# Optimization experiments

Hardware: AMD Instinct MI355X
Metric: run time of the kernel (lower is better)

Reference implementation:

```python
import jax, jax.numpy as jnp
import numpy as np

B = 256            # user batch size
D = 64             # embedding_dim
NR_USERS = 100000
NR_ITEMS = 10000
HID = 32


def _mlp_params(key, in_dim):
    # Keras Dense default: glorot_uniform weights, zero bias
    dims = [in_dim, HID, HID, HID, 1]
    ws, bs = [], []
    for i in range(4):
        key, k = jax.random.split(key)
        lim = np.sqrt(6.0 / (dims[i] + dims[i + 1])).astype(np.float32)
        ws.append(jax.random.uniform(k, (dims[i], dims[i + 1]), jnp.float32, -lim, lim))
        bs.append(jnp.zeros((dims[i + 1],), jnp.float32))
    return ws, bs


def setup_inputs() -> dict:
    key = jax.random.key(0)
    ks = jax.random.split(key, 6)
    users = jax.random.randint(ks[0], (B,), 0, NR_USERS)
    user_emb = jax.random.normal(ks[1], (NR_USERS, D), jnp.float32)
    item_emb = jax.random.normal(ks[2], (NR_ITEMS, D), jnp.float32)
    inp = {"users": users, "user_emb": user_emb, "item_emb": item_emb}
    for name, k, in_dim in (("l", ks[3], 2 * D), ("r", ks[4], 2 * D), ("p", ks[5], D)):
        ws, bs = _mlp_params(k, in_dim)
        for i in range(4):
            inp[f"{name}w{i}"] = ws[i]
            inp[f"{name}b{i}"] = bs[i]
    return inp


def _pair_head(eu, ie, ws, bs):
    # Faithful to: concat([tile(eu),[1,I,1]], tile(ie,[B,1,1])) @ W0 + b0
    # concat @ W0 == eu @ W0[:D] + ie @ W0[D:]  (avoids materializing [B,I,2D])
    h = jax.nn.relu((eu @ ws[0][:D])[:, None, :] + (ie @ ws[0][D:])[None, :, :] + bs[0])
    h = jax.nn.relu(h @ ws[1] + bs[1])
    h = jax.nn.relu(h @ ws[2] + bs[2])
    return jax.nn.sigmoid(h @ ws[3] + bs[3])[..., 0]  # [B, I]


def _item_head(x, ws, bs):
    h = jax.nn.relu(x @ ws[0] + bs[0])
    h = jax.nn.relu(h @ ws[1] + bs[1])
    h = jax.nn.relu(h @ ws[2] + bs[2])
    return jax.nn.sigmoid(h @ ws[3] + bs[3])[..., 0]  # [I]


def reference(users, user_emb, item_emb,
              lw0, lb0, lw1, lb1, lw2, lb2, lw3, lb3,
              rw0, rb0, rw1, rb1, rw2, rb2, rw3, rb3,
              pw0, pb0, pw1, pb1, pw2, pb2, pw3, pb3):
    eu = user_emb[users]  # [B, D]
    likes = _pair_head(eu, item_emb, [lw0, lw1, lw2, lw3], [lb0, lb1, lb2, lb3])
    rated = _pair_head(eu, item_emb, [rw0, rw1, rw2, rw3], [rb0, rb1, rb2, rb3])
    popular = _item_head(item_emb, [pw0, pw1, pw2, pw3], [pb0, pb1, pb2, pb3])
    # tf.keras.losses.cosine_similarity returns NEGATIVE cosine similarity,
    # so sim = (1 + (-cos)) / 2 = (1 - cos) / 2
    n = eu * jax.lax.rsqrt(jnp.maximum(jnp.sum(eu * eu, -1, keepdims=True), 1e-12))
    cos = n @ n.T  # [B, B]
    user_sim = (1.0 - cos) / 2.0
    return likes, user_sim, rated, popular
```

## Files before the change

### kernel.cpp

```cpp
#include <hip/hip_runtime.h>
#include <hip/hip_bf16.h>

#define NB 256
#define D 64
#define NI 10000

typedef __attribute__((ext_vector_type(8))) short bf16x8;
typedef __attribute__((ext_vector_type(16))) float f32x16;

union PK8 { unsigned u[4]; bf16x8 v; };

static constexpr int WS_AL  = 0;
static constexpr int WS_AR  = 8192;
static constexpr int WS_N   = 16384;
static constexpr int WS_CL  = 32768;
static constexpr int WS_CR  = 352768;
static constexpr int WS_TAB = 672768;

static constexpr long OUT_LIKES = 0;
static constexpr long OUT_SIM   = 2560000;
static constexpr long OUT_RATED = 2625536;
static constexpr long OUT_POP   = 5185536;

__device__ __forceinline__ unsigned pkbf(float a, float b) {
    unsigned r;
    asm("v_cvt_pk_bf16_f32 %0, %1, %2" : "=v"(r) : "v"(a), "v"(b));
    return r;
}
__device__ __forceinline__ float relu(float x) { return fmaxf(x, 0.f); }

struct A4 { float4 a0, a1, a2, a3; };
__device__ __forceinline__ A4 ldA(const float* p) {
    A4 r;
    r.a0 = *(const float4*)p;        r.a1 = *(const float4*)(p + 4);
    r.a2 = *(const float4*)(p + 16); r.a3 = *(const float4*)(p + 20);
    return r;
}

__global__ __launch_bounds__(256) void k_prep(
        const int* __restrict__ users, const float* __restrict__ uemb,
        const float* __restrict__ iemb,
        const float* __restrict__ lw0, const float* __restrict__ lb0,
        const float* __restrict__ rw0, const float* __restrict__ rb0,
        const float* __restrict__ lw1, const float* __restrict__ lb1,
        const float* __restrict__ lw2, const float* __restrict__ lb2,
        const float* __restrict__ lw3, const float* __restrict__ lb3,
        const float* __restrict__ rw1, const float* __restrict__ rb1,
        const float* __restrict__ rw2, const float* __restrict__ rb2,
        const float* __restrict__ rw3, const float* __restrict__ rb3,
        const float* __restrict__ pw0, const float* __restrict__ pb0,
        const float* __restrict__ pw1, const float* __restrict__ pb1,
        const float* __restrict__ pw2, const float* __restrict__ pb2,
        const float* __restrict__ pw3, const float* __restrict__ pb3,
        float* __restrict__ ws, float* __restrict__ out) {
    int bx = blockIdx.x, t = threadIdx.x;
    if (bx == 0) {
        if (t >= 128) return;
        int head = t >> 6, lane = t & 63;
        int pr = lane & 31, hi = lane >> 5;
        const float* W1 = head ? rw1 : lw1; const float* B1 = head ? rb1 : lb1;
        const float* W2 = head ? rw2 : lw2; const float* B2 = head ? rb2 : lb2;
        const float* w3 = head ? rw3 : lw3; const float* b3 = head ? rb3 : lb3;
        PK8 w1a, w1b, w2a, w2b, w3a, w3b;
        #pragma unroll
        for (int j = 0; j < 4; ++j) {
            int k0 = 8 * hi + 2 * j;
            w1a.u[j] = pkbf(W1[k0 * 32 + pr],        W1[(k0 + 1) * 32 + pr]);
            w1b.u[j] = pkbf(W1[(16 + k0) * 32 + pr], W1[(17 + k0) * 32 + pr]);
            int fa = ((2 * j) & 3) + 8 * ((2 * j) >> 2) + 4 * hi;
            int fb = ((2 * j + 1) & 3) + 8 * ((2 * j + 1) >> 2) + 4 * hi;
            w2a.u[j] = pkbf(W2[fa * 32 + pr],        W2[fb * 32 + pr]);
            w2b.u[j] = pkbf(W2[(fa + 16) * 32 + pr], W2[(fb + 16) * 32 + pr]);
            w3a.u[j] = pkbf(w3[fa],                  w3[fb]);
            w3b.u[j] = pkbf(w3[fa + 16],             w3[fb + 16]);
        }
        float* base = ws + WS_TAB + head * 3600;
        ((uint4*)base)[0 * 64 + lane] = *(uint4*)&w1a;
        ((uint4*)base)[1 * 64 + lane] = *(uint4*)&w1b;
        ((uint4*)base)[2 * 64 + lane] = *(uint4*)&w2a;
        ((uint4*)base)[3 * 64 + lane] = *(uint4*)&w2b;
        ((uint4*)base)[4 * 64 + lane] = *(uint4*)&w3a;
        ((uint4*)base)[5 * 64 + lane] = *(uint4*)&w3b;
        #pragma unroll
        for (int q = 0; q < 4; ++q) {
            float4 v1, v2;
            #pragma unroll
            for (int e = 0; e < 4; ++e) {
                int r = 4 * q + e;
                int f = (r & 3) + 8 * (r >> 2) + 4 * hi;
                ((float*)&v1)[e] = B1[f];
                ((float*)&v2)[e] = B2[f];
            }
            ((float4*)base)[(6 + q) * 64 + lane]  = v1;
            ((float4*)base)[(10 + q) * 64 + lane] = v2;
        }
        if (lane == 0) base[14 * 256] = b3[0];
    } else if (bx < 80) {
        int wv = t >> 6, lane = t & 63;
        int w = (bx - 1) * 4 + wv;
        if (w >= 313) return;
        int i0 = w * 32;
        int pr = lane & 31, hi = lane >> 5;
        int crow = i0 + pr; if (crow > NI - 1) crow = NI - 1;
        const float4* xr = (const float4*)(iemb + (long)crow * D);
        PK8 xm[4], w0f[4];
        #pragma unroll
        for (int m = 0; m < 4; ++m) {
            float4 xa = xr[4 * m + 2 * hi];
            float4 xb = xr[4 * m + 2 * hi + 1];
            xm[m].u[0] = pkbf(xa.x, xa.y); xm[m].u[1] = pkbf(xa.z, xa.w);
            xm[m].u[2] = pkbf(xb.x, xb.y); xm[m].u[3] = pkbf(xb.z, xb.w);
            #pragma unroll
            for (int j = 0; j < 4; ++j) {
                int r0 = 16 * m + 8 * hi + 2 * j;
                w0f[m].u[j] = pkbf(pw0[r0 * 32 + pr], pw0[(r0 + 1) * 32 + pr]);
            }
        }
        PK8 w1a, w1b, w2a, w2b, w3a, w3b;
        f32x16 b0i, b1i, b2i, b3i;
        #pragma unroll
        for (int j = 0; j < 4; ++j) {
            int fa = ((2 * j) & 3) + 8 * ((2 * j) >> 2) + 4 * hi;
            int fb = ((2 * j + 1) & 3) + 8 * ((2 * j + 1) >> 2) + 4 * hi;
            w1a.u[j] = pkbf(pw1[fa * 32 + pr],        pw1[fb * 32 + pr]);
            w1b.u[j] = pkbf(pw1[(fa + 16) * 32 + pr], pw1[(fb + 16) * 32 + pr]);
            w2a.u[j] = pkbf(pw2[fa * 32 + pr],        pw2[fb * 32 + pr]);
            w2b.u[j] = pkbf(pw2[(fa + 16) * 32 + pr], pw2[(fb + 16) * 32 + pr]);
            w3a.u[j] = pkbf(pw3[fa],                  pw3[fb]);
            w3b.u[j] = pkbf(pw3[fa + 16],             pw3[fb + 16]);
        }
        float b3s = pb3[0];
        #pragma unroll
        for (int r = 0; r < 16; ++r) {
            int f = (r & 3) + 8 * (r >> 2) + 4 * hi;
            b0i[r] = pb0[f]; b1i[r] = pb1[f]; b2i[r] = pb2[f]; b3i[r] = b3s;
        }
        f32x16 acc = b0i;
        acc = __builtin_amdgcn_mfma_f32_32x32x16_bf16(w0f[0].v, xm[0].v, acc, 0, 0, 0);
        acc = __builtin_amdgcn_mfma_f32_32x32x16_bf16(w0f[1].v, xm[1].v, acc, 0, 0, 0);
        acc = __builtin_amdgcn_mfma_f32_32x32x16_bf16(w0f[2].v, xm[2].v, acc, 0, 0, 0);
        acc = __builtin_amdgcn_mfma_f32_32x32x16_bf16(w0f[3].v, xm[3].v, acc, 0, 0, 0);
        PK8 g0, g1;
        #pragma unroll
        for (int j = 0; j < 4; ++j) {
            g0.u[j] = pkbf(relu(acc[2 * j]),     relu(acc[2 * j + 1]));
            g1.u[j] = pkbf(relu(acc[8 + 2 * j]), relu(acc[9 + 2 * j]));
        }
        f32x16 a1 = b1i;
        a1 = __builtin_amdgcn_mfma_f32_32x32x16_bf16(w1a.v, g0.v, a1, 0, 0, 0);
        a1 = __builtin_amdgcn_mfma_f32_32x32x16_bf16(w1b.v, g1.v, a1, 0, 0, 0);
        #pragma unroll
        for (int j = 0; j < 4; ++j) {
            g0.u[j] = pkbf(relu(a1[2 * j]),     relu(a1[2 * j + 1]));
            g1.u[j] = pkbf(relu(a1[8 + 2 * j]), relu(a1[9 + 2 * j]));
        }
        f32x16 a2 = b2i;
        a2 = __builtin_amdgcn_mfma_f32_32x32x16_bf16(w2a.v, g0.v, a2, 0, 0, 0);
        a2 = __builtin_amdgcn_mfma_f32_32x32x16_bf16(w2b.v, g1.v, a2, 0, 0, 0);
        #pragma unroll
        for (int j = 0; j < 4; ++j) {
            g0.u[j] = pkbf(relu(a2[2 * j]),     relu(a2[2 * j + 1]));
            g1.u[j] = pkbf(relu(a2[8 + 2 * j]), relu(a2[9 + 2 * j]));
        }
        f32x16 a3 = b3i;
        a3 = __builtin_amdgcn_mfma_f32_32x32x16_bf16(w3a.v, g0.v, a3, 0, 0, 0);
        a3 = __builtin_amdgcn_mfma_f32_32x32x16_bf16(w3b.v, g1.v, a3, 0, 0, 0);
        float o = 1.f / (1.f + __expf(-a3[0]));
        if (hi == 0 && i0 + pr < NI) out[OUT_POP + i0 + pr] = o;
    } else if (bx < 80 + 1250) {
        int i0 = (bx - 80) * 8;
        __shared__ float xs[8][D];
        for (int idx = t; idx < 8 * D; idx += 256) {
            int it = idx >> 6, d = idx & 63; int gi = i0 + it;
            xs[it][d] = (gi < NI) ? iemb[(long)gi * D + d] : 0.f;
        }
        __syncthreads();
        int it = t >> 5, j = t & 31; int gi = i0 + it;
        float al = 0.f, ar = 0.f;
        #pragma unroll
        for (int d = 0; d < D; ++d) {
            float x = xs[it][d];
            al += x * lw0[(D + d) * 32 + j];
            ar += x * rw0[(D + d) * 32 + j];
        }
        if (gi < NI) { ws[WS_CL + gi * 32 + j] = al; ws[WS_CR + gi * 32 + j] = ar; }
    } else {
        __shared__ float es[4][D];
        int ug = t >> 6, tt = t & 63;
        int b = (bx - 1330) * 4 + ug;
        int u = users[b];
        float e = uemb[(long)u * D + tt];
        float s = e * e;
        #pragma unroll
        for (int off = 32; off; off >>= 1) s += __shfl_down(s, off);
        s = __shfl(s, 0);
        ws[WS_N + b * D + tt] = e * rsqrtf(fmaxf(s, 1e-12f));
        es[ug][tt] = e;
        __syncthreads();
        const float* W0 = (tt < 32) ? lw0 : rw0;
        const float* bb = (tt < 32) ? lb0 : rb0;
        int j = tt & 31;
        float acc = bb[j];
        #pragma unroll
        for (int d = 0; d < D; ++d) acc += es[ug][d] * W0[d * 32 + j];
        ws[((tt < 32) ? WS_AL : WS_AR) + b * 32 + j] = acc;
    }
}

__global__ __launch_bounds__(256) void k_main(
        const float* __restrict__ ws, float* __restrict__ out) {
    __shared__ float nb[D];
    int bx = blockIdx.x, t = threadIdx.x;
    if (bx < 2504) {
        int head = bx & 1;
        int ug = (bx >> 1) & 3;
        int ib = bx >> 3;
        int i0 = ib * 32;
        int a_off = head ? WS_AR : WS_AL;
        int c_off = head ? WS_CR : WS_CL;
        float* ob = out + (head ? OUT_RATED : OUT_LIKES);

        int lane = t & 63, wv = t >> 6;
        int pr = lane & 31, hi = lane >> 5;
        int u0 = ug * 64 + wv * 16;

        const float* base = ws + WS_TAB + head * 3600;
        PK8 w1a, w1b, w2a, w2b, w3a, w3b;
        *(uint4*)&w1a = ((const uint4*)base)[0 * 64 + lane];
        *(uint4*)&w1b = ((const uint4*)base)[1 * 64 + lane];
        *(uint4*)&w2a = ((const uint4*)base)[2 * 64 + lane];
        *(uint4*)&w2b = ((const uint4*)base)[3 * 64 + lane];
        *(uint4*)&w3a = ((const uint4*)base)[4 * 64 + lane];
        *(uint4*)&w3b = ((const uint4*)base)[5 * 64 + lane];
        f32x16 binit1, binit2, binit3;
        #pragma unroll
        for (int q = 0; q < 4; ++q) {
            float4 v1 = ((const float4*)base)[(6 + q) * 64 + lane];
            float4 v2 = ((const float4*)base)[(10 + q) * 64 + lane];
            binit1[4*q+0] = v1.x; binit1[4*q+1] = v1.y;
            binit1[4*q+2] = v1.z; binit1[4*q+3] = v1.w;
            binit2[4*q+0] = v2.x; binit2[4*q+1] = v2.y;
            binit2[4*q+2] = v2.z; binit2[4*q+3] = v2.w;
        }
        float b3s = base[14 * 256];
        #pragma unroll
        for (int r = 0; r < 16; ++r) binit3[r] = b3s;

        int crow = i0 + pr; if (crow > NI - 1) crow = NI - 1;
        const float* cp = ws + c_off + (long)crow * 32 + 8 * hi;
        float4 c0 = *(const float4*)cp;
        float4 c1 = *(const float4*)(cp + 4);
        float4 c2 = *(const float4*)(cp + 16);
        float4 c3 = *(const float4*)(cp + 20);

        bool valid = (hi == 0) && (i0 + pr < NI);
        float* op = ob + (long)u0 * NI + i0 + pr;
        const float* ap = ws + a_off + 8 * hi + (long)u0 * 32;

        A4 aA = ldA(ap);
        A4 aB = ldA(ap + 32);

        for (int u = 0; u < 16; u += 2) {
            PK8 xA0, xA1, xB0, xB1;
            xA0.u[0] = pkbf(relu(aA.a0.x + c0.x), relu(aA.a0.y + c0.y));
            xA0.u[1] = pkbf(relu(aA.a0.z + c0.z), relu(aA.a0.w + c0.w));
            xA0.u[2] = pkbf(relu(aA.a1.x + c1.x), relu(aA.a1.y + c1.y));
            xA0.u[3] = pkbf(relu(aA.a1.z + c1.z), relu(aA.a1.w + c1.w));
            xA1.u[0] = pkbf(relu(aA.a2.x + c2.x), relu(aA.a2.y + c2.y));
            xA1.u[1] = pkbf(relu(aA.a2.z + c2.z), relu(aA.a2.w + c2.w));
            xA1.u[2] = pkbf(relu(aA.a3.x + c3.x), relu(aA.a3.y + c3.y));
            xA1.u[3] = pkbf(relu(aA.a3.z + c3.z), relu(aA.a3.w + c3.w));
            xB0.u[0] = pkbf(relu(aB.a0.x + c0.x), relu(aB.a0.y + c0.y));
            xB0.u[1] = pkbf(relu(aB.a0.z + c0.z), relu(aB.a0.w + c0.w));
            xB0.u[2] = pkbf(relu(aB.a1.x + c1.x), relu(aB.a1.y + c1.y));
            xB0.u[3] = pkbf(relu(aB.a1.z + c1.z), relu(aB.a1.w + c1.w));
            xB1.u[0] = pkbf(relu(aB.a2.x + c2.x), relu(aB.a2.y + c2.y));
            xB1.u[1] = pkbf(relu(aB.a2.z + c2.z), relu(aB.a2.w + c2.w));
            xB1.u[2] = pkbf(relu(aB.a3.x + c3.x), relu(aB.a3.y + c3.y));
            xB1.u[3] = pkbf(relu(aB.a3.z + c3.z), relu(aB.a3.w + c3.w));
            f32x16 accA = binit1;
            accA = __builtin_amdgcn_mfma_f32_32x32x16_bf16(w1a.v, xA0.v, accA, 0, 0, 0);
            f32x16 accB = binit1;
            accB = __builtin_amdgcn_mfma_f32_32x32x16_bf16(w1a.v, xB0.v, accB, 0, 0, 0);
            accA = __builtin_amdgcn_mfma_f32_32x32x16_bf16(w1b.v, xA1.v, accA, 0, 0, 0);
            accB = __builtin_amdgcn_mfma_f32_32x32x16_bf16(w1b.v, xB1.v, accB, 0, 0, 0);
            int un = (u < 14) ? (u + 2) : u;
            aA = ldA(ap + (long)un * 32);
            aB = ldA(ap + (long)(un + 1) * 32);
            PK8 hA0, hA1, hB0, hB1;
            #pragma unroll
            for (int j = 0; j < 4; ++j) {
                hA0.u[j] = pkbf(relu(accA[2 * j]),     relu(accA[2 * j + 1]));
                hA1.u[j] = pkbf(relu(accA[8 + 2 * j]), relu(accA[9 + 2 * j]));
                hB0.u[j] = pkbf(relu(accB[2 * j]),     relu(accB[2 * j + 1]));
                hB1.u[j] = pkbf(relu(accB[8 + 2 * j]), relu(accB[9 + 2 * j]));
            }
            f32x16 acc2A = binit2;
            acc2A = __builtin_amdgcn_mfma_f32_32x32x16_bf16(w2a.v, hA0.v, acc2A, 0, 0, 0);
            f32x16 acc2B = binit2;
            acc2B = __builtin_amdgcn_mfma_f32_32x32x16_bf16(w2a.v, hB0.v, acc2B, 0, 0, 0);
            acc2A = __builtin_amdgcn_mfma_f32_32x32x16_bf16(w2b.v, hA1.v, acc2A, 0, 0, 0);
            acc2B = __builtin_amdgcn_mfma_f32_32x32x16_bf16(w2b.v, hB1.v, acc2B, 0, 0, 0);
            PK8 gA0, gA1, gB0, gB1;
            #pragma unroll
            for (int j = 0; j < 4; ++j) {
                gA0.u[j] = pkbf(relu(acc2A[2 * j]),     relu(acc2A[2 * j + 1]));
                gA1.u[j] = pkbf(relu(acc2A[8 + 2 * j]), relu(acc2A[9 + 2 * j]));
                gB0.u[j] = pkbf(relu(acc2B[2 * j]),     relu(acc2B[2 * j + 1]));
                gB1.u[j] = pkbf(relu(acc2B[8 + 2 * j]), relu(acc2B[9 + 2 * j]));
            }
            f32x16 acc3A = binit3;
            acc3A = __builtin_amdgcn_mfma_f32_32x32x16_bf16(w3a.v, gA0.v, acc3A, 0, 0, 0);
            f32x16 acc3B = binit3;
            acc3B = __builtin_amdgcn_mfma_f32_32x32x16_bf16(w3a.v, gB0.v, acc3B, 0, 0, 0);
            acc3A = __builtin_amdgcn_mfma_f32_32x32x16_bf16(w3b.v, gA1.v, acc3A, 0, 0, 0);
            acc3B = __builtin_amdgcn_mfma_f32_32x32x16_bf16(w3b.v, gB1.v, acc3B, 0, 0, 0);
            float oA = 1.f / (1.f + __expf(-acc3A[0]));
            float oB = 1.f / (1.f + __expf(-acc3B[0]));
            if (valid) { op[0] = oA; op[NI] = oB; }
            op += 2 * NI;
        }
    } else {
        int b = bx - 2504;
        if (t < D) nb[t] = ws[WS_N + b * D + t];
        __syncthreads();
        const float4* nj = (const float4*)(ws + WS_N + t * D);
        float acc = 0.f;
        #pragma unroll
        for (int d4 = 0; d4 < 16; ++d4) {
            float4 v = nj[d4];
            acc += nb[4*d4+0] * v.x + nb[4*d4+1] * v.y
                 + nb[4*d4+2] * v.z + nb[4*d4+3] * v.w;
        }
        out[OUT_SIM + (long)b * 256 + t] = (1.f - acc) * 0.5f;
    }
}

extern "C" void kernel_launch(void* const* d_in, const int* in_sizes, int n_in,
                              void* d_out, int out_size, void* d_ws, size_t ws_size,
                              hipStream_t stream) {
    const int*   users = (const int*)d_in[0];
    const float* uemb  = (const float*)d_in[1];
    const float* iemb  = (const float*)d_in[2];
    const float *lw0 = (const float*)d_in[3],  *lb0 = (const float*)d_in[4];
    const float *lw1 = (const float*)d_in[5],  *lb1 = (const float*)d_in[6];
    const float *lw2 = (const float*)d_in[7],  *lb2 = (const float*)d_in[8];
    const float *lw3 = (const float*)d_in[9],  *lb3 = (const float*)d_in[10];
    const float *rw0 = (const float*)d_in[11], *rb0 = (const float*)d_in[12];
    const float *rw1 = (const float*)d_in[13], *rb1 = (const float*)d_in[14];
    const float *rw2 = (const float*)d_in[15], *rb2 = (const float*)d_in[16];
    const float *rw3 = (const float*)d_in[17], *rb3 = (const float*)d_in[18];
    const float *pw0 = (const float*)d_in[19], *pb0 = (const float*)d_in[20];
    const float *pw1 = (const float*)d_in[21], *pb1 = (const float*)d_in[22];
    const float *pw2 = (const float*)d_in[23], *pb2 = (const float*)d_in[24];
    const float *pw3 = (const float*)d_in[25], *pb3 = (const float*)d_in[26];
    float* ws = (float*)d_ws;
    float* out = (float*)d_out;

    k_prep<<<1394, 256, 0, stream>>>(users, uemb, iemb,
                                     lw0, lb0, rw0, rb0,
                                     lw1, lb1, lw2, lb2, lw3, lb3,
                                     rw1, rb1, rw2, rb2, rw3, rb3,
                                     pw0, pb0, pw1, pb1, pw2, pb2, pw3, pb3,
                                     ws, out);
    k_main<<<2760, 256, 0, stream>>>(ws, out);
}
```

Measured before the change: 80.11 us.

## Stage MLP weight/bias table in LDS and process one user per iteration

Copies the per-head weight and bias table into shared memory once per block. Bias accumulator initial values are now reloaded from LDS each iteration instead of being held in registers, and the b3 bias is stored pre-broadcast in the table. The main loop drops from two users per iteration to one and sets launch bounds to 4 blocks per SM, cutting register pressure to raise occupancy. In exchange it loses the two-way interleaved MFMA ILP and adds 18KB of LDS per block plus extra LDS reads every iteration.

```diff
diff --git a/kernel.cpp b/kernel.cpp
--- a/kernel.cpp
+++ b/kernel.cpp
@@ -9,6 +9,7 @@
 typedef __attribute__((ext_vector_type(16))) float f32x16;
 
 union PK8 { unsigned u[4]; bf16x8 v; };
+union F16Q { f32x16 v; float4 q[4]; };
 
 static constexpr int WS_AL  = 0;
 static constexpr int WS_AR  = 8192;
@@ -74,7 +75,7 @@
             w3a.u[j] = pkbf(w3[fa],                  w3[fb]);
             w3b.u[j] = pkbf(w3[fa + 16],             w3[fb + 16]);
         }
-        float* base = ws + WS_TAB + head * 3600;
+        float* base = ws + WS_TAB + head * 4608;
         ((uint4*)base)[0 * 64 + lane] = *(uint4*)&w1a;
         ((uint4*)base)[1 * 64 + lane] = *(uint4*)&w1b;
         ((uint4*)base)[2 * 64 + lane] = *(uint4*)&w2a;
@@ -94,7 +95,10 @@
             ((float4*)base)[(6 + q) * 64 + lane]  = v1;
             ((float4*)base)[(10 + q) * 64 + lane] = v2;
         }
-        if (lane == 0) base[14 * 256] = b3[0];
+        float b3v = b3[0];
+        float4 bs; bs.x = b3v; bs.y = b3v; bs.z = b3v; bs.w = b3v;
+        #pragma unroll
+        for (int q = 0; q < 4; ++q) ((float4*)base)[(14 + q) * 64 + lane] = bs;
     } else if (bx < 80) {
         int wv = t >> 6, lane = t & 63;
         int w = (bx - 1) * 4 + wv;
@@ -207,9 +211,9 @@
     }
 }
 
-__global__ __launch_bounds__(256) void k_main(
+__global__ __launch_bounds__(256, 4) void k_main(
         const float* __restrict__ ws, float* __restrict__ out) {
-    __shared__ float nb[D];
+    __shared__ float tabf[4608];
     int bx = blockIdx.x, t = threadIdx.x;
     if (bx < 2504) {
         int head = bx & 1;
@@ -220,31 +224,26 @@
         int c_off = head ? WS_CR : WS_CL;
         float* ob = out + (head ? OUT_RATED : OUT_LIKES);
 
+        {
+            const float4* g = (const float4*)(ws + WS_TAB + head * 4608);
+            float4* l = (float4*)tabf;
+            for (int idx = t; idx < 1152; idx += 256) l[idx] = g[idx];
+        }
+        __syncthreads();
+
         int lane = t & 63, wv = t >> 6;
         int pr = lane & 31, hi = lane >> 5;
         int u0 = ug * 64 + wv * 16;
 
-        const float* base = ws + WS_TAB + head * 3600;
+        const uint4*  tu = (const uint4*)tabf;
+        const float4* tq = (const float4*)tabf;
         PK8 w1a, w1b, w2a, w2b, w3a, w3b;
-        *(uint4*)&w1a = ((const uint4*)base)[0 * 64 + lane];
-        *(uint4*)&w1b = ((const uint4*)base)[1 * 64 + lane];
-        *(uint4*)&w2a = ((const uint4*)base)[2 * 64 + lane];
-        *(uint4*)&w2b = ((const uint4*)base)[3 * 64 + lane];
-        *(uint4*)&w3a = ((const uint4*)base)[4 * 64 + lane];
-        *(uint4*)&w3b = ((const uint4*)base)[5 * 64 + lane];
-        f32x16 binit1, binit2, binit3;
-        #pragma unroll
-        for (int q = 0; q < 4; ++q) {
-            float4 v1 = ((const float4*)base)[(6 + q) * 64 + lane];
-            float4 v2 = ((const float4*)base)[(10 + q) * 64 + lane];
-            binit1[4*q+0] = v1.x; binit1[4*q+1] = v1.y;
-            binit1[4*q+2] = v1.z; binit1[4*q+3] = v1.w;
-            binit2[4*q+0] = v2.x; binit2[4*q+1] = v2.y;
-            binit2[4*q+2] = v2.z; binit2[4*q+3] = v2.w;
-        }
-        float b3s = base[14 * 256];
-        #pragma unroll
-        for (int r = 0; r < 16; ++r) binit3[r] = b3s;
+        *(uint4*)&w1a = tu[0 * 64 + lane];
+        *(uint4*)&w1b = tu[1 * 64 + lane];
+        *(uint4*)&w2a = tu[2 * 64 + lane];
+        *(uint4*)&w2b = tu[3 * 64 + lane];
+        *(uint4*)&w3a = tu[4 * 64 + lane];
+        *(uint4*)&w3b = tu[5 * 64 + lane];
 
         int crow = i0 + pr; if (crow > NI - 1) crow = NI - 1;
         const float* cp = ws + c_off + (long)crow * 32 + 8 * hi;
@@ -257,80 +256,62 @@
         float* op = ob + (long)u0 * NI + i0 + pr;
         const float* ap = ws + a_off + 8 * hi + (long)u0 * 32;
 
-        A4 aA = ldA(ap);
-        A4 aB = ldA(ap + 32);
-
-        for (int u = 0; u < 16; u += 2) {
-            PK8 xA0, xA1, xB0, xB1;
-            xA0.u[0] = pkbf(relu(aA.a0.x + c0.x), relu(aA.a0.y + c0.y));
-            xA0.u[1] = pkbf(relu(aA.a0.z + c0.z), relu(aA.a0.w + c0.w));
-            xA0.u[2] = pkbf(relu(aA.a1.x + c1.x), relu(aA.a1.y + c1.y));
-            xA0.u[3] = pkbf(relu(aA.a1.z + c1.z), relu(aA.a1.w + c1.w));
-            xA1.u[0] = pkbf(relu(aA.a2.x + c2.x), relu(aA.a2.y + c2.y));
-            xA1.u[1] = pkbf(relu(aA.a2.z + c2.z), relu(aA.a2.w + c2.w));
-            xA1.u[2] = pkbf(relu(aA.a3.x + c3.x), relu(aA.a3.y + c3.y));
-            xA1.u[3] = pkbf(relu(aA.a3.z + c3.z), relu(aA.a3.w + c3.w));
-            xB0.u[0] = pkbf(relu(aB.a0.x + c0.x), relu(aB.a0.y + c0.y));
-            xB0.u[1] = pkbf(relu(aB.a0.z + c0.z), relu(aB.a0.w + c0.w));
-            xB0.u[2] = pkbf(relu(aB.a1.x + c1.x), relu(aB.a1.y + c1.y));
-            xB0.u[3] = pkbf(relu(aB.a1.z + c1.z), relu(aB.a1.w + c1.w));
-            xB1.u[0] = pkbf(relu(aB.a2.x + c2.x), relu(aB.a2.y + c2.y));
-            xB1.u[1] = pkbf(relu(aB.a2.z + c2.z), relu(aB.a2.w + c2.w));
-            xB1.u[2] = pkbf(relu(aB.a3.x + c3.x), relu(aB.a3.y + c3.y));
-            xB1.u[3] = pkbf(relu(aB.a3.z + c3.z), relu(aB.a3.w + c3.w));
-            f32x16 accA = binit1;
-            accA = __builtin_amdgcn_mfma_f32_32x32x16_bf16(w1a.v, xA0.v, accA, 0, 0, 0);
-            f32x16 accB = binit1;
-            accB = __builtin_amdgcn_mfma_f32_32x32x16_bf16(w1a.v, xB0.v, accB, 0, 0, 0);
-            accA = __builtin_amdgcn_mfma_f32_32x32x16_bf16(w1b.v, xA1.v, accA, 0, 0, 0);
-            accB = __builtin_amdgcn_mfma_f32_32x32x16_bf16(w1b.v, xB1.v, accB, 0, 0, 0);
-            int un = (u < 14) ? (u + 2) : u;
-            aA = ldA(ap + (long)un * 32);
-            aB = ldA(ap + (long)(un + 1) * 32);
-            PK8 hA0, hA1, hB0, hB1;
+        A4 a = ldA(ap);
+        for (int u = 0; u < 16; ++u) {
+            A4 an = a;
+            if (u < 15) an = ldA(ap + (long)(u + 1) * 32);
+            PK8 x0, x1;
+            x0.u[0] = pkbf(relu(a.a0.x + c0.x), relu(a.a0.y + c0.y));
+            x0.u[1] = pkbf(relu(a.a0.z + c0.z), relu(a.a0.w + c0.w));
+            x0.u[2] = pkbf(relu(a.a1.x + c1.x), relu(a.a1.y + c1.y));
+            x0.u[3] = pkbf(relu(a.a1.z + c1.z), relu(a.a1.w + c1.w));
+            x1.u[0] = pkbf(relu(a.a2.x + c2.x), relu(a.a2.y + c2.y));
+            x1.u[1] = pkbf(relu(a.a2.z + c2.z), relu(a.a2.w + c2.w));
+            x1.u[2] = pkbf(relu(a.a3.x + c3.x), relu(a.a3.y + c3.y));
+            x1.u[3] = pkbf(relu(a.a3.z + c3.z), relu(a.a3.w + c3.w));
+            F16Q acc;
+            acc.q[0] = tq[6 * 64 + lane]; acc.q[1] = tq[7 * 64 + lane];
+            acc.q[2] = tq[8 * 64 + lane]; acc.q[3] = tq[9 * 64 + lane];
+            acc.v = __builtin_amdgcn_mfma_f32_32x32x16_bf16(w1a.v, x0.v, acc.v, 0, 0, 0);
+            acc.v = __builtin_amdgcn_mfma_f32_32x32x16_bf16(w1b.v, x1.v, acc.v, 0, 0, 0);
+            PK8 h0, h1;
             #pragma unroll
             for (int j = 0; j < 4; ++j) {
-                hA0.u[j] = pkbf(relu(accA[2 * j]),     relu(accA[2 * j + 1]));
-                hA1.u[j] = pkbf(relu(accA[8 + 2 * j]), relu(accA[9 + 2 * j]));
-                hB0.u[j] = pkbf(relu(accB[2 * j]),     relu(accB[2 * j + 1]));
-                hB1.u[j] = pkbf(relu(accB[8 + 2 * j]), relu(accB[9 + 2 * j]));
+                h0.u[j] = pkbf(relu(acc.v[2 * j]),     relu(acc.v[2 * j + 1]));
+                h1.u[j] = pkbf(relu(acc.v[8 + 2 * j]), relu(acc.v[9 + 2 * j]));
             }
-            f32x16 acc2A = binit2;
-            acc2A = __builtin_amdgcn_mfma_f32_32x32x16_bf16(w2a.v, hA0.v, acc2A, 0, 0, 0);
-            f32x16 acc2B = binit2;
-            acc2B = __builtin_amdgcn_mfma_f32_32x32x16_bf16(w2a.v, hB0.v, acc2B, 0, 0, 0);
-            acc2A = __builtin_amdgcn_mfma_f32_32x32x16_bf16(w2b.v, hA1.v, acc2A, 0, 0, 0);
-            acc2B = __builtin_amdgcn_mfma_f32_32x32x16_bf16(w2b.v, hB1.v, acc2B, 0, 0, 0);
-            PK8 gA0, gA1, gB0, gB1;
+            F16Q acc2;
+            acc2.q[0] = tq[10 * 64 + lane]; acc2.q[1] = tq[11 * 64 + lane];
+            acc2.q[2] = tq[12 * 64 + lane]; acc2.q[3] = tq[13 * 64 + lane];
+            acc2.v = __builtin_amdgcn_mfma_f32_32x32x16_bf16(w2a.v, h0.v, acc2.v, 0, 0, 0);
+            acc2.v = __builtin_amdgcn_mfma_f32_32x32x16_bf16(w2b.v, h1.v, acc2.v, 0, 0, 0);
+            PK8 g0, g1;
             #pragma unroll
             for (int j = 0; j < 4; ++j) {
-                gA0.u[j] = pkbf(relu(acc2A[2 * j]),     relu(acc2A[2 * j + 1]));
-                gA1.u[j] = pkbf(relu(acc2A[8 + 2 * j]), relu(acc2A[9 + 2 * j]));
-                gB0.u[j] = pkbf(relu(acc2B[2 * j]),     relu(acc2B[2 * j + 1]));
-                gB1.u[j] = pkbf(relu(acc2B[8 + 2 * j]), relu(acc2B[9 + 2 * j]));
+                g0.u[j] = pkbf(relu(acc2.v[2 * j]),     relu(acc2.v[2 * j + 1]));
+                g1.u[j] = pkbf(relu(acc2.v[8 + 2 * j]), relu(acc2.v[9 + 2 * j]));
             }
-            f32x16 acc3A = binit3;
-            acc3A = __builtin_amdgcn_mfma_f32_32x32x16_bf16(w3a.v, gA0.v, acc3A, 0, 0, 0);
-            f32x16 acc3B = binit3;
-            acc3B = __builtin_amdgcn_mfma_f32_32x32x16_bf16(w3a.v, gB0.v, acc3B, 0, 0, 0);
-            acc3A = __builtin_amdgcn_mfma_f32_32x32x16_bf16(w3b.v, gA1.v, acc3A, 0, 0, 0);
-            acc3B = __builtin_amdgcn_mfma_f32_32x32x16_bf16(w3b.v, gB1.v, acc3B, 0, 0, 0);
-            float oA = 1.f / (1.f + __expf(-acc3A[0]));
-            float oB = 1.f / (1.f + __expf(-acc3B[0]));
-            if (valid) { op[0] = oA; op[NI] = oB; }
-            op += 2 * NI;
+            F16Q acc3;
+            acc3.q[0] = tq[14 * 64 + lane]; acc3.q[1] = tq[15 * 64 + lane];
+            acc3.q[2] = tq[16 * 64 + lane]; acc3.q[3] = tq[17 * 64 + lane];
+            acc3.v = __builtin_amdgcn_mfma_f32_32x32x16_bf16(w3a.v, g0.v, acc3.v, 0, 0, 0);
+            acc3.v = __builtin_amdgcn_mfma_f32_32x32x16_bf16(w3b.v, g1.v, acc3.v, 0, 0, 0);
+            float o = 1.f / (1.f + __expf(-acc3.v[0]));
+            if (valid) *op = o;
+            op += NI;
+            a = an;
         }
     } else {
         int b = bx - 2504;
-        if (t < D) nb[t] = ws[WS_N + b * D + t];
+        if (t < D) tabf[t] = ws[WS_N + b * D + t];
         __syncthreads();
         const float4* nj = (const float4*)(ws + WS_N + t * D);
         float acc = 0.f;
         #pragma unroll
         for (int d4 = 0; d4 < 16; ++d4) {
             float4 v = nj[d4];
-            acc += nb[4*d4+0] * v.x + nb[4*d4+1] * v.y
-                 + nb[4*d4+2] * v.z + nb[4*d4+3] * v.w;
+            acc += tabf[4*d4+0] * v.x + tabf[4*d4+1] * v.y
+                 + tabf[4*d4+2] * v.z + tabf[4*d4+3] * v.w;
         }
         out[OUT_SIM + (long)b * 256 + t] = (1.f - acc) * 0.5f;
     }
```

After: 69.26 us. 1.16x faster.
